# Kernel tuning notes

Measured on AMD Instinct MI355X. Metric: run time of the kernel, lower is better.

## Reference

```python
import jax, jax.numpy as jnp
import numpy as np

B, T, C, H = 4, 4096, 512, 64

def setup_inputs() -> dict:
    key = jax.random.key(0)
    kx, kk, kq, kv = jax.random.split(key, 4)
    return {
        "x": jax.random.normal(kx, (B, T, C), dtype=jnp.float32),
        "Wk": jax.random.normal(kk, (C, H), dtype=jnp.float32) * (C ** -0.5),
        "Wq": jax.random.normal(kq, (C, H), dtype=jnp.float32) * (C ** -0.5),
        "Wv": jax.random.normal(kv, (C, H), dtype=jnp.float32) * (C ** -0.5),
    }

def reference(x, Wk, Wq, Wv):
    # x: [B, T, C]; bias-free projections to head_size H
    k = x @ Wk  # [B, T, H]
    q = x @ Wq  # [B, T, H]
    v = x @ Wv  # [B, T, H]
    channels = x.shape[-1]
    # NOTE: original scales by channels**-0.5 (embedding dim), not head_size
    scale = jnp.asarray(channels, x.dtype) ** -0.5
    wei = jnp.einsum("bth,bsh->bts", q, k) * scale  # [B, T, T]
    t = x.shape[1]
    causal = jnp.tril(jnp.ones((t, t), dtype=bool))
    wei = jnp.where(causal, wei, -jnp.inf)
    wei = jax.nn.softmax(wei, axis=-1)
    out = jnp.einsum("bts,bsh->bth", wei, v)  # [B, T, H]
    return out
```

## Files before the change

### kernel.cpp

```cpp
#include <hip/hip_runtime.h>


typedef __attribute__((ext_vector_type(8))) __bf16 bf16x8;
typedef __attribute__((ext_vector_type(8))) unsigned short u16x8;
typedef __attribute__((ext_vector_type(4))) float f32x4;

#define B_ 4
#define T_ 4096
#define C_ 512
#define H_ 64
#define BT (B_ * T_)

#define QSCALE (0.04419417382415922f * 1.4426950408889634f)

__device__ __forceinline__ unsigned short f2bf(float f) {
    unsigned int u = __builtin_bit_cast(unsigned int, f);
    u += 0x7fffu + ((u >> 16) & 1u);
    return (unsigned short)(u >> 16);
}

__device__ __forceinline__ unsigned int pkbf(float hi, float lo) {
    return __builtin_amdgcn_perm(__builtin_bit_cast(unsigned int, hi),
                                 __builtin_bit_cast(unsigned int, lo), 0x07060302u);
}

__device__ __forceinline__ f32x4 mfma16(bf16x8 a, bf16x8 b, f32x4 c) {
    return __builtin_amdgcn_mfma_f32_16x16x32_bf16(a, b, c, 0, 0, 0);
}

__global__ __launch_bounds__(256) void wt_kernel(const float* __restrict__ Wk,
                                                 const float* __restrict__ Wq,
                                                 const float* __restrict__ Wv,
                                                 unsigned short* __restrict__ Wtp) {
    int gid = blockIdx.x * 256 + threadIdx.x;
    int fidx = gid >> 9;
    int li = gid & 511;
    int lane = li >> 3, j = li & 7;
    int m3 = fidx / 64;
    int rem = fidx & 63;
    int nt = rem >> 4, kc = rem & 15;
    int h = nt * 16 + (lane & 15);
    int c = kc * 32 + (lane >> 4) * 8 + j;
    const float* W = (m3 == 0) ? Wk : ((m3 == 1) ? Wq : Wv);
    Wtp[gid] = f2bf(W[c * H_ + h]);
}

__global__ __launch_bounds__(256, 3) void proj_kernel(const float* __restrict__ x,
                                                      const unsigned short* __restrict__ Wtp,
                                                      unsigned short* __restrict__ Kf,
                                                      unsigned short* __restrict__ Qf,
                                                      unsigned short* __restrict__ Vf) {
    __shared__ __align__(16) char smem[2 * 64 * 52 * 4];
    float* Mg = (float*)smem;
    unsigned short* Ks_l = (unsigned short*)smem;
    unsigned short* Qs_l = Ks_l + 32 * 68;
    unsigned short* Vt_l = Qs_l + 32 * 68;

    const int tid = threadIdx.x;
    const int t0 = blockIdx.x * 32;
    const int wave = tid >> 6;
    const int ws = wave & 1;
    const int wh = wave >> 1;
    const int lane = tid & 63;
    const int lane15 = lane & 15;
    const int quad = lane >> 4;

    f32x4 acc[12];
#pragma unroll
    for (int i = 0; i < 12; ++i) acc[i] = (f32x4){0.f, 0.f, 0.f, 0.f};

    const float* xrow = x + (long)(t0 + ws * 16 + lane15) * C_;
    const unsigned short* wbase = Wtp + lane * 8;

    bf16x8 wf[12];
    float4 xa0, xa1;
    {
        const int kc0 = wh * 8;
        xa0 = *(const float4*)(xrow + kc0 * 32 + quad * 8);
        xa1 = *(const float4*)(xrow + kc0 * 32 + quad * 8 + 4);
#pragma unroll
        for (int i = 0; i < 12; ++i)
            wf[i] = *(const bf16x8*)(wbase + ((i * 16 + kc0) << 9));
    }

#pragma unroll
    for (int kk = 0; kk < 8; ++kk) {
        const int kc = wh * 8 + kk;
        u16x8 t;
        t[0] = f2bf(xa0.x); t[1] = f2bf(xa0.y); t[2] = f2bf(xa0.z); t[3] = f2bf(xa0.w);
        t[4] = f2bf(xa1.x); t[5] = f2bf(xa1.y); t[6] = f2bf(xa1.z); t[7] = f2bf(xa1.w);
        bf16x8 a = __builtin_bit_cast(bf16x8, t);
        if (kk < 7) {
            xa0 = *(const float4*)(xrow + (kc + 1) * 32 + quad * 8);
            xa1 = *(const float4*)(xrow + (kc + 1) * 32 + quad * 8 + 4);
        }
#pragma unroll
        for (int i = 0; i < 12; ++i) {
            acc[i] = mfma16(a, wf[i], acc[i]);
            if (kk < 7)
                wf[i] = *(const bf16x8*)(wbase + ((i * 16 + kc + 1) << 9));
        }
    }

    if (wh == 1) {
        float* mg = Mg + (ws * 64 + lane) * 52;
#pragma unroll
        for (int i = 0; i < 12; ++i) *(f32x4*)(mg + i * 4) = acc[i];
    }
    __syncthreads();
    if (wh == 0) {
        const float* mg = Mg + (ws * 64 + lane) * 52;
#pragma unroll
        for (int i = 0; i < 12; ++i) acc[i] += *(const f32x4*)(mg + i * 4);
    }
    __syncthreads();

    if (wh == 0) {
#pragma unroll
        for (int nt = 0; nt < 4; ++nt) {
            int col = nt * 16 + lane15;
#pragma unroll
            for (int r = 0; r < 4; ++r) {
                int row_l = ws * 16 + quad * 4 + r;
                Ks_l[row_l * 68 + col] = f2bf(acc[0 * 4 + nt][r]);
                Qs_l[row_l * 68 + col] = f2bf(acc[1 * 4 + nt][r] * QSCALE);
                Vt_l[col * 34 + row_l] = f2bf(acc[2 * 4 + nt][r]);
            }
        }
    }
    __syncthreads();

    const int b = t0 >> 12;
    const int tloc = t0 & 4095;
    const int st = wave >> 1, kk = wave & 1;
    const long gs = (long)(b * 256 + (tloc >> 4) + st);
    bf16x8 kv = *(const bf16x8*)&Ks_l[(st * 16 + lane15) * 68 + kk * 32 + quad * 8];
    *(bf16x8*)&Kf[(gs * 2 + kk) * 512 + lane * 8] = kv;
    bf16x8 qv = *(const bf16x8*)&Qs_l[(st * 16 + lane15) * 68 + kk * 32 + quad * 8];
    *(bf16x8*)&Qf[(gs * 2 + kk) * 512 + lane * 8] = qv;
    const int hf = wave;
    const int vkk = (tloc >> 5) & 1;
    bf16x8 vv = *(const bf16x8*)&Vt_l[(hf * 16 + lane15) * 34 + quad * 8];
    const long sb = (long)(b * 64 + (tloc >> 6));
    *(bf16x8*)&Vf[(sb * 8 + hf * 2 + vkk) * 512 + lane * 8] = vv;
}

#define PSP 72

__global__ __launch_bounds__(256, 3) void attn_kernel(const unsigned short* __restrict__ Qf,
                                                      const unsigned short* __restrict__ Kf,
                                                      const unsigned short* __restrict__ Vf,
                                                      float* __restrict__ Op,
                                                      float* __restrict__ lp,
                                                      float* __restrict__ out) {
    __shared__ __align__(16) unsigned short Ps[4 * 16 * PSP];

    const int tid = threadIdx.x;
    const int wave = tid >> 6;
    const int lane = tid & 63;
    const int lane15 = lane & 15;
    const int quad = lane >> 4;
    const int b = blockIdx.y;

    const int z = 159 - blockIdx.x;
    int g, zb;
    if (z < 16)      { g = 0; zb = 0; }
    else if (z < 48) { g = 1; zb = 16; }
    else if (z < 96) { g = 2; zb = 48; }
    else             { g = 3; zb = 96; }
    const int idx = z - zb;
    const int qt = g * 16 + idx / (g + 1);
    const int chunk = idx % (g + 1);
    const int ntt = min(16, qt + 1 - chunk * 16);
    const int t0k = chunk * 16;

    const long gs_q = (long)(b * 256 + qt * 4 + wave);
    const unsigned short* qb = Qf + gs_q * 1024 + lane * 8;
    const bf16x8 qf0 = *(const bf16x8*)qb;
    const bf16x8 qf1 = *(const bf16x8*)(qb + 512);

    f32x4 o_acc[4];
    float l_acc = 0.f;
#pragma unroll
    for (int hf = 0; hf < 4; ++hf) o_acc[hf] = (f32x4){0.f, 0.f, 0.f, 0.f};

    unsigned short* pw = Ps + wave * 16 * PSP;

    bf16x8 kf[8], vf[8];
    {
        const unsigned short* kb = Kf + (long)(b * 256 + t0k * 4) * 1024 + lane * 8;
        const unsigned short* vb = Vf + (long)(b * 64 + t0k) * 4096 + lane * 8;
#pragma unroll
        for (int ct = 0; ct < 4; ++ct) {
            kf[ct * 2 + 0] = *(const bf16x8*)(kb + ct * 1024);
            kf[ct * 2 + 1] = *(const bf16x8*)(kb + ct * 1024 + 512);
        }
#pragma unroll
        for (int f = 0; f < 8; ++f) vf[f] = *(const bf16x8*)(vb + f * 512);
    }

    for (int t = 0; t < ntt; ++t) {
        const int kc = t0k + t;
        const bool more = (t + 1 < ntt);
        const unsigned short* kbn = Kf + (long)(b * 256 + (kc + 1) * 4) * 1024 + lane * 8;
        const unsigned short* vbn = Vf + (long)(b * 64 + kc + 1) * 4096 + lane * 8;

        f32x4 st[4];
#pragma unroll
        for (int ct = 0; ct < 4; ++ct) {
            f32x4 zz = (f32x4){0.f, 0.f, 0.f, 0.f};
            zz = mfma16(kf[ct * 2 + 0], qf0, zz);
            zz = mfma16(kf[ct * 2 + 1], qf1, zz);
            st[ct] = zz;
        }

        if (more) {
#pragma unroll
            for (int ct = 0; ct < 4; ++ct) {
                kf[ct * 2 + 0] = *(const bf16x8*)(kbn + ct * 1024);
                kf[ct * 2 + 1] = *(const bf16x8*)(kbn + ct * 1024 + 512);
            }
        }

        if (kc == qt) {
            const int qg = wave * 16 + lane15;
#pragma unroll
            for (int ct = 0; ct < 4; ++ct) {
                const int sb = ct * 16 + quad * 4;
#pragma unroll
                for (int r = 0; r < 4; ++r)
                    if (sb + r > qg) st[ct][r] = -3.0e38f;
            }
        }

#pragma unroll
        for (int ct = 0; ct < 4; ++ct)
#pragma unroll
            for (int r = 0; r < 4; ++r) {
                float p = __builtin_amdgcn_exp2f(st[ct][r]);
                st[ct][r] = p;
                l_acc += p;
            }

#pragma unroll
        for (int ct = 0; ct < 4; ++ct) {
            unsigned int w0 = pkbf(st[ct][1], st[ct][0]);
            unsigned int w1 = pkbf(st[ct][3], st[ct][2]);
            *(uint2*)&pw[lane15 * PSP + ct * 16 + quad * 4] = make_uint2(w0, w1);
        }

        bf16x8 pa0 = *(const bf16x8*)&pw[lane15 * PSP + quad * 8];
        bf16x8 pa1 = *(const bf16x8*)&pw[lane15 * PSP + 32 + quad * 8];
#pragma unroll
        for (int hf = 0; hf < 4; ++hf) {
            o_acc[hf] = mfma16(pa0, vf[hf * 2 + 0], o_acc[hf]);
            o_acc[hf] = mfma16(pa1, vf[hf * 2 + 1], o_acc[hf]);
        }

        if (more) {
#pragma unroll
            for (int f = 0; f < 8; ++f) vf[f] = *(const bf16x8*)(vbn + f * 512);
        }
    }

    l_acc += __shfl_xor(l_acc, 16);
    l_acc += __shfl_xor(l_acc, 32);

    if ((qt >> 4) == 0) {
        float linv[4];
#pragma unroll
        for (int r = 0; r < 4; ++r) linv[r] = 1.0f / __shfl(l_acc, quad * 4 + r);
        float* o = out + ((long)b * T_ + qt * 64 + wave * 16) * H_;
#pragma unroll
        for (int hf = 0; hf < 4; ++hf)
#pragma unroll
            for (int r = 0; r < 4; ++r)
                o[(quad * 4 + r) * H_ + hf * 16 + lane15] = o_acc[hf][r] * linv[r];
    } else {
        const long pbase = ((long)(b * 64 + qt) * 4 + chunk) * 64;
        if (quad == 0) lp[pbase + wave * 16 + lane15] = l_acc;
        float* op = Op + (pbase + wave * 16) * 64;
#pragma unroll
        for (int hf = 0; hf < 4; ++hf)
#pragma unroll
            for (int r = 0; r < 4; ++r)
                op[(quad * 4 + r) * 64 + hf * 16 + lane15] = o_acc[hf][r];
    }
}

__global__ __launch_bounds__(256) void merge_kernel(const float* __restrict__ Op,
                                                    const float* __restrict__ lp,
                                                    float* __restrict__ out) {
    const int qt = 16 + blockIdx.x;
    const int b = blockIdx.y;
    const int nc = 1 + (qt >> 4);
    const int tid = threadIdx.x;
    const int row = tid >> 2;
    const int seg = (tid & 3) << 4;

    const long base = (long)(b * 64 + qt) * 4;
    float l = 0.f;
    f32x4 a[4];
#pragma unroll
    for (int j = 0; j < 4; ++j) a[j] = (f32x4){0.f, 0.f, 0.f, 0.f};

    for (int c = 0; c < nc; ++c) {
        l += lp[(base + c) * 64 + row];
        const float* op = Op + ((base + c) * 64 + row) * 64 + seg;
#pragma unroll
        for (int j = 0; j < 4; ++j) a[j] += *(const f32x4*)(op + j * 4);
    }
    const float inv = 1.0f / l;
    float* o = out + ((long)b * T_ + qt * 64 + row) * H_ + seg;
#pragma unroll
    for (int j = 0; j < 4; ++j) *(f32x4*)(o + j * 4) = a[j] * inv;
}

extern "C" void kernel_launch(void* const* d_in, const int* in_sizes, int n_in,
                              void* d_out, int out_size, void* d_ws, size_t ws_size,
                              hipStream_t stream) {
    const float* x  = (const float*)d_in[0];
    const float* Wk = (const float*)d_in[1];
    const float* Wq = (const float*)d_in[2];
    const float* Wv = (const float*)d_in[3];
    float* out = (float*)d_out;

    char* ws = (char*)d_ws;
    unsigned short* Kf  = (unsigned short*)(ws);
    unsigned short* Qf  = (unsigned short*)(ws + (2u << 20));
    unsigned short* Vf  = (unsigned short*)(ws + (4u << 20));
    unsigned short* Wtp = (unsigned short*)(ws + (6u << 20));
    float* Op = (float*)(ws + (8u << 20));
    float* lp = (float*)(ws + (24u << 20));

    wt_kernel<<<384, 256, 0, stream>>>(Wk, Wq, Wv, Wtp);
    proj_kernel<<<BT / 32, 256, 0, stream>>>(x, Wtp, Kf, Qf, Vf);
    attn_kernel<<<dim3(160, B_), 256, 0, stream>>>(Qf, Kf, Vf, Op, lp, out);
    merge_kernel<<<dim3(48, B_), 256, 0, stream>>>(Op, lp, out);
}
```

Before: 120.5 us.

## Fuse split-K merge into attention kernel via atomic last-block counter

Drops the separate merge kernel. Each attention block that writes a partial result now bumps a per-query-tile atomic counter, and the last-arriving block reduces all partials and writes the normalized output. The counter array is zeroed inside wt_kernel. It also replaces the scalar row-sum accumulation with a vector accumulate that is reduced after the loop. This saves one kernel launch and its tail, at the cost of thread fences, an atomic and a serial merge tail inside some attention blocks.

```diff
diff --git a/kernel.cpp b/kernel.cpp
--- a/kernel.cpp
+++ b/kernel.cpp
@@ -31,7 +31,9 @@
 __global__ __launch_bounds__(256) void wt_kernel(const float* __restrict__ Wk,
                                                  const float* __restrict__ Wq,
                                                  const float* __restrict__ Wv,
-                                                 unsigned short* __restrict__ Wtp) {
+                                                 unsigned short* __restrict__ Wtp,
+                                                 int* __restrict__ cnt) {
+    if (blockIdx.x == 0) cnt[threadIdx.x] = 0;
     int gid = blockIdx.x * 256 + threadIdx.x;
     int fidx = gid >> 9;
     int li = gid & 511;
@@ -152,8 +154,10 @@
                                                       const unsigned short* __restrict__ Vf,
                                                       float* __restrict__ Op,
                                                       float* __restrict__ lp,
+                                                      int* __restrict__ cnt,
                                                       float* __restrict__ out) {
     __shared__ __align__(16) unsigned short Ps[4 * 16 * PSP];
+    __shared__ int do_merge;
 
     const int tid = threadIdx.x;
     const int wave = tid >> 6;
@@ -180,7 +184,7 @@
     const bf16x8 qf1 = *(const bf16x8*)(qb + 512);
 
     f32x4 o_acc[4];
-    float l_acc = 0.f;
+    f32x4 l_vec = (f32x4){0.f, 0.f, 0.f, 0.f};
 #pragma unroll
     for (int hf = 0; hf < 4; ++hf) o_acc[hf] = (f32x4){0.f, 0.f, 0.f, 0.f};
 
@@ -234,13 +238,12 @@
         }
 
 #pragma unroll
-        for (int ct = 0; ct < 4; ++ct)
-#pragma unroll
-            for (int r = 0; r < 4; ++r) {
-                float p = __builtin_amdgcn_exp2f(st[ct][r]);
-                st[ct][r] = p;
-                l_acc += p;
-            }
+        for (int ct = 0; ct < 4; ++ct) {
+#pragma unroll
+            for (int r = 0; r < 4; ++r)
+                st[ct][r] = __builtin_amdgcn_exp2f(st[ct][r]);
+            l_vec += st[ct];
+        }
 
 #pragma unroll
         for (int ct = 0; ct < 4; ++ct) {
@@ -263,6 +266,7 @@
         }
     }
 
+    float l_acc = (l_vec[0] + l_vec[1]) + (l_vec[2] + l_vec[3]);
     l_acc += __shfl_xor(l_acc, 16);
     l_acc += __shfl_xor(l_acc, 32);
 
@@ -277,6 +281,7 @@
             for (int r = 0; r < 4; ++r)
                 o[(quad * 4 + r) * H_ + hf * 16 + lane15] = o_acc[hf][r] * linv[r];
     } else {
+        const int nc = 1 + (qt >> 4);
         const long pbase = ((long)(b * 64 + qt) * 4 + chunk) * 64;
         if (quad == 0) lp[pbase + wave * 16 + lane15] = l_acc;
         float* op = Op + (pbase + wave * 16) * 64;
@@ -285,35 +290,35 @@
 #pragma unroll
             for (int r = 0; r < 4; ++r)
                 op[(quad * 4 + r) * 64 + hf * 16 + lane15] = o_acc[hf][r];
-    }
-}
-
-__global__ __launch_bounds__(256) void merge_kernel(const float* __restrict__ Op,
-                                                    const float* __restrict__ lp,
-                                                    float* __restrict__ out) {
-    const int qt = 16 + blockIdx.x;
-    const int b = blockIdx.y;
-    const int nc = 1 + (qt >> 4);
-    const int tid = threadIdx.x;
-    const int row = tid >> 2;
-    const int seg = (tid & 3) << 4;
-
-    const long base = (long)(b * 64 + qt) * 4;
-    float l = 0.f;
-    f32x4 a[4];
-#pragma unroll
-    for (int j = 0; j < 4; ++j) a[j] = (f32x4){0.f, 0.f, 0.f, 0.f};
-
-    for (int c = 0; c < nc; ++c) {
-        l += lp[(base + c) * 64 + row];
-        const float* op = Op + ((base + c) * 64 + row) * 64 + seg;
-#pragma unroll
-        for (int j = 0; j < 4; ++j) a[j] += *(const f32x4*)(op + j * 4);
-    }
-    const float inv = 1.0f / l;
-    float* o = out + ((long)b * T_ + qt * 64 + row) * H_ + seg;
-#pragma unroll
-    for (int j = 0; j < 4; ++j) *(f32x4*)(o + j * 4) = a[j] * inv;
+
+        __threadfence();
+        if (tid == 0) {
+            int old = atomicAdd(&cnt[b * 64 + qt], 1);
+            do_merge = (old == nc - 1) ? 1 : 0;
+        }
+        __syncthreads();
+
+        if (do_merge) {
+            __threadfence();
+            const int row = tid >> 2;
+            const int seg = (tid & 3) << 4;
+            const long base = (long)(b * 64 + qt) * 4;
+            float l = 0.f;
+            f32x4 a[4];
+#pragma unroll
+            for (int j = 0; j < 4; ++j) a[j] = (f32x4){0.f, 0.f, 0.f, 0.f};
+            for (int c = 0; c < nc; ++c) {
+                l += lp[(base + c) * 64 + row];
+                const float* opr = Op + ((base + c) * 64 + row) * 64 + seg;
+#pragma unroll
+                for (int j = 0; j < 4; ++j) a[j] += *(const f32x4*)(opr + j * 4);
+            }
+            const float inv = 1.0f / l;
+            float* o = out + ((long)b * T_ + qt * 64 + row) * H_ + seg;
+#pragma unroll
+            for (int j = 0; j < 4; ++j) *(f32x4*)(o + j * 4) = a[j] * inv;
+        }
+    }
 }
 
 extern "C" void kernel_launch(void* const* d_in, const int* in_sizes, int n_in,
@@ -330,11 +335,11 @@
     unsigned short* Qf  = (unsigned short*)(ws + (2u << 20));
     unsigned short* Vf  = (unsigned short*)(ws + (4u << 20));
     unsigned short* Wtp = (unsigned short*)(ws + (6u << 20));
+    int* cnt = (int*)(ws + (7u << 20));
     float* Op = (float*)(ws + (8u << 20));
     float* lp = (float*)(ws + (24u << 20));
 
-    wt_kernel<<<384, 256, 0, stream>>>(Wk, Wq, Wv, Wtp);
+    wt_kernel<<<384, 256, 0, stream>>>(Wk, Wq, Wv, Wtp, cnt);
     proj_kernel<<<BT / 32, 256, 0, stream>>>(x, Wtp, Kf, Qf, Vf);
-    attn_kernel<<<dim3(160, B_), 256, 0, stream>>>(Qf, Kf, Vf, Op, lp, out);
-    merge_kernel<<<dim3(48, B_), 256, 0, stream>>>(Op, lp, out);
-}
+    attn_kernel<<<dim3(160, B_), 256, 0, stream>>>(Qf, Kf, Vf, Op, lp, cnt, out);
+}
```

New measurement: 219.7 us. +82.3%, slower.
